# Kernel tuning notes

Hardware: AMD Instinct MI355X
Metric: run time of the kernel (lower is better)

Reference implementation:

```python
import jax, jax.numpy as jnp
import numpy as np

B, C, H, W = 256, 3, 224, 224
BRIGHT, CONTR, SATUR, HUE = 0.4, 0.4, 0.4, 0.1
ERASE_P = 0.25
PI = 3.14159


def _forward(x, flip_u, bj_u, cj_u, sj_u, hue_u, erase_u, area_u, aspect_u,
             top_u, left_u, erase_noise, mean, std):
    # uint8 -> float [0,1]
    xf = x.astype(jnp.float32) / 255.0
    # random horizontal flip (flip when rand > 0.5)
    flip = (flip_u > 0.5)[:, None, None, None]
    xf = jnp.where(flip, xf[..., ::-1], xf)
    # color jitter: brightness
    b_fac = 1.0 + (bj_u * 2.0 - 1.0) * BRIGHT
    xf = xf * b_fac
    # contrast
    c_fac = 1.0 + (cj_u * 2.0 - 1.0) * CONTR
    gray = xf.mean(axis=1, keepdims=True)
    xf = c_fac * xf + (1.0 - c_fac) * gray
    # saturation
    s_fac = 1.0 + (sj_u * 2.0 - 1.0) * SATUR
    gray = xf.mean(axis=1, keepdims=True)
    xf = s_fac * xf + (1.0 - s_fac) * gray
    # hue rotation
    h_fac = (hue_u * 2.0 - 1.0) * HUE * 0.5
    cos_h = jnp.cos(h_fac * PI)[:, None, None, None]
    sin_h = jnp.sin(h_fac * PI)[:, None, None, None]
    r, g, b = xf[:, 0:1], xf[:, 1:2], xf[:, 2:3]
    gray = (r + g + b) / 3.0
    xf = jnp.concatenate([
        gray + (r - gray) * cos_h + (g - b) * sin_h * 0.5,
        gray + (g - gray) * cos_h + (b - r) * sin_h * 0.5,
        gray + (b - gray) * cos_h + (r - g) * sin_h * 0.5,
    ], axis=1)
    xf = jnp.clip(xf, 0.0, 1.0)
    # normalize
    xf = (xf - mean) / std
    # vectorized random erasing
    area = float(H * W)
    target_area = (0.02 + area_u * (0.33 - 0.02)) * area          # [B]
    aspect = 0.3 + aspect_u * (3.3 - 0.3)                         # [B]
    h_e = jnp.round(jnp.sqrt(target_area * aspect)).astype(jnp.int32)
    w_e = jnp.round(jnp.sqrt(target_area / aspect)).astype(jnp.int32)
    apply = (erase_u < ERASE_P) & (h_e < H) & (w_e < W)           # [B]
    top = jnp.floor(top_u * jnp.maximum(H - h_e + 1, 1).astype(jnp.float32)).astype(jnp.int32)
    left = jnp.floor(left_u * jnp.maximum(W - w_e + 1, 1).astype(jnp.float32)).astype(jnp.int32)
    rows = jnp.arange(H)[None, :, None]   # [1,H,1]
    cols = jnp.arange(W)[None, None, :]   # [1,1,W]
    t = top[:, None, None]; l = left[:, None, None]
    he = h_e[:, None, None]; we = w_e[:, None, None]
    box = (rows >= t) & (rows < t + he) & (cols >= l) & (cols < l + we)  # [B,H,W]
    mask = (box & apply[:, None, None])[:, None, :, :]            # [B,1,H,W]
    xf = jnp.where(mask, erase_noise, xf)
    return xf


def setup_inputs() -> dict:
    key = jax.random.key(0)
    ks = jax.random.split(key, 14)
    return {
        "x": jax.random.randint(ks[0], (B, C, H, W), 0, 256, dtype=jnp.int32),
        "flip_u": jax.random.uniform(ks[1], (B,)),
        "bj_u": jax.random.uniform(ks[2], (B, 1, 1, 1)),
        "cj_u": jax.random.uniform(ks[3], (B, 1, 1, 1)),
        "sj_u": jax.random.uniform(ks[4], (B, 1, 1, 1)),
        "hue_u": jax.random.uniform(ks[5], (B,)),
        "erase_u": jax.random.uniform(ks[6], (B,)),
        "area_u": jax.random.uniform(ks[7], (B,)),
        "aspect_u": jax.random.uniform(ks[8], (B,)),
        "top_u": jax.random.uniform(ks[9], (B,)),
        "left_u": jax.random.uniform(ks[10], (B,)),
        "erase_noise": jax.random.normal(ks[11], (B, C, H, W), dtype=jnp.float32),
        "mean": jnp.array([0.485, 0.456, 0.406], dtype=jnp.float32).reshape(1, 3, 1, 1),
        "std": jnp.array([0.229, 0.224, 0.225], dtype=jnp.float32).reshape(1, 3, 1, 1),
    }


def reference(x, flip_u, bj_u, cj_u, sj_u, hue_u, erase_u, area_u, aspect_u,
              top_u, left_u, erase_noise, mean, std):
    return _forward(x, flip_u, bj_u, cj_u, sj_u, hue_u, erase_u, area_u,
                    aspect_u, top_u, left_u, erase_noise, mean, std)
```

## Files before the change

### kernel.cpp

```cpp
#include <hip/hip_runtime.h>
#include <math.h>

#define NB 256
#define NC 3
#define NH 224
#define NW 224
#define HW (NH * NW)
#define CHW (NC * HW)
#define GP 4
#define NT 256
#define WGR (NW / GP)
#define GPI (HW / GP)
#define BPI (GPI / NT)

struct __align__(16) Params {
    float b255;
    float k1;
    float k2;
    int   flip, apply, top, left, he, we;
};

__device__ inline void compute_params(int b,
    const float* __restrict__ flip_u, const float* __restrict__ bj_u,
    const float* __restrict__ cj_u,   const float* __restrict__ sj_u,
    const float* __restrict__ hue_u,  const float* __restrict__ erase_u,
    const float* __restrict__ area_u, const float* __restrict__ aspect_u,
    const float* __restrict__ top_u,  const float* __restrict__ left_u,
    Params* p)
{
#pragma clang fp contract(off)
    p->flip  = (flip_u[b] > 0.5f) ? 1 : 0;
    float b_fac = 1.0f + (bj_u[b] * 2.0f - 1.0f) * 0.4f;
    float c_fac = 1.0f + (cj_u[b] * 2.0f - 1.0f) * 0.4f;
    float s_fac = 1.0f + (sj_u[b] * 2.0f - 1.0f) * 0.4f;
    float h_fac = (hue_u[b] * 2.0f - 1.0f) * 0.1f * 0.5f;
    float ang   = h_fac * 3.14159f;
    float cs = c_fac * s_fac;
    p->b255 = b_fac * (1.0f / 255.0f);
    p->k1   = cs * cosf(ang);
    p->k2   = cs * sinf(ang) * 0.5f;

    float ta     = (0.02f + area_u[b] * 0.31f) * (float)HW;
    float aspect = 0.3f + aspect_u[b] * 3.0f;
    int he = (int)rintf(sqrtf(ta * aspect));
    int we = (int)rintf(sqrtf(ta / aspect));
    int apply = (erase_u[b] < 0.25f) && (he < NH) && (we < NW);
    int th = NH - he + 1; if (th < 1) th = 1;
    int tw = NW - we + 1; if (tw < 1) tw = 1;
    p->top  = (int)floorf(top_u[b]  * (float)th);
    p->left = (int)floorf(left_u[b] * (float)tw);
    p->he = he; p->we = we; p->apply = apply;
}

__global__ __launch_bounds__(NT) void aug_kernel(
    const int*   __restrict__ x,
    const float* __restrict__ flip_u, const float* __restrict__ bj_u,
    const float* __restrict__ cj_u,   const float* __restrict__ sj_u,
    const float* __restrict__ hue_u,  const float* __restrict__ erase_u,
    const float* __restrict__ area_u, const float* __restrict__ aspect_u,
    const float* __restrict__ top_u,  const float* __restrict__ left_u,
    const float* __restrict__ noise,  const float* __restrict__ mean,
    const float* __restrict__ stdv,
    float* __restrict__ out)
{
    __shared__ Params sp;
    __shared__ float sinv[3], smi[3];

    const int bimg = blockIdx.x / BPI;
    if (threadIdx.x == 0) {
        compute_params(bimg, flip_u, bj_u, cj_u, sj_u, hue_u, erase_u,
                       area_u, aspect_u, top_u, left_u, &sp);
        #pragma unroll
        for (int c = 0; c < 3; ++c) {
            float inv = 1.0f / stdv[c];
            sinv[c] = inv;
            smi[c]  = mean[c] * inv;
        }
    }
    __syncthreads();

    const int r  = (blockIdx.x % BPI) * NT + threadIdx.x;
    const int h  = r / WGR;
    const int w4 = (r - h * WGR) * GP;

    const int base  = bimg * CHW + h * NW;
    const int srcw4 = sp.flip ? (NW - GP - w4) : w4;

    int4 xi0 = *(const int4*)(x + base          + srcw4);
    int4 xi1 = *(const int4*)(x + base + HW     + srcw4);
    int4 xi2 = *(const int4*)(x + base + 2*HW   + srcw4);

    const float b255 = sp.b255, k1 = sp.k1, k2 = sp.k2;
    const float i0 = sinv[0], i1 = sinv[1], i2 = sinv[2];
    const float mi0 = smi[0], mi1 = smi[1], mi2 = smi[2];
    const float third = 1.0f / 3.0f;
    const int   flip = sp.flip;

    float v[3][GP];
    {
        const int* p0 = (const int*)&xi0;
        const int* p1 = (const int*)&xi1;
        const int* p2 = (const int*)&xi2;
        #pragma unroll
        for (int i = 0; i < GP; ++i) {
            const int src = flip ? (GP - 1 - i) : i;
            float r_ = (float)p0[src] * b255;
            float g_ = (float)p1[src] * b255;
            float b_ = (float)p2[src] * b255;

            float gray = (r_ + g_ + b_) * third;
            float rn = fmaf(k2, g_ - b_, fmaf(k1, r_ - gray, gray));
            float gn = fmaf(k2, b_ - r_, fmaf(k1, g_ - gray, gray));
            float bn = fmaf(k2, r_ - g_, fmaf(k1, b_ - gray, gray));

            rn = fminf(fmaxf(rn, 0.0f), 1.0f);
            gn = fminf(fmaxf(gn, 0.0f), 1.0f);
            bn = fminf(fmaxf(bn, 0.0f), 1.0f);

            v[0][i] = fmaf(rn, i0, -mi0);
            v[1][i] = fmaf(gn, i1, -mi1);
            v[2][i] = fmaf(bn, i2, -mi2);
        }
    }

    const bool rowin = sp.apply && (h >= sp.top) && (h < sp.top + sp.he);
    if (rowin) {
        #pragma unroll
        for (int i = 0; i < GP; ++i) {
            const int col = w4 + i;
            if (col >= sp.left && col < sp.left + sp.we) {
                v[0][i] = noise[base          + col];
                v[1][i] = noise[base + HW     + col];
                v[2][i] = noise[base + 2*HW   + col];
            }
        }
    }

    *(float4*)(out + base          + w4) = make_float4(v[0][0], v[0][1], v[0][2], v[0][3]);
    *(float4*)(out + base + HW     + w4) = make_float4(v[1][0], v[1][1], v[1][2], v[1][3]);
    *(float4*)(out + base + 2*HW   + w4) = make_float4(v[2][0], v[2][1], v[2][2], v[2][3]);
}

extern "C" void kernel_launch(void* const* d_in, const int* in_sizes, int n_in,
                              void* d_out, int out_size, void* d_ws, size_t ws_size,
                              hipStream_t stream) {
    const int*   x        = (const int*)  d_in[0];
    const float* flip_u   = (const float*)d_in[1];
    const float* bj_u     = (const float*)d_in[2];
    const float* cj_u     = (const float*)d_in[3];
    const float* sj_u     = (const float*)d_in[4];
    const float* hue_u    = (const float*)d_in[5];
    const float* erase_u  = (const float*)d_in[6];
    const float* area_u   = (const float*)d_in[7];
    const float* aspect_u = (const float*)d_in[8];
    const float* top_u    = (const float*)d_in[9];
    const float* left_u   = (const float*)d_in[10];
    const float* noise    = (const float*)d_in[11];
    const float* mean     = (const float*)d_in[12];
    const float* stdv     = (const float*)d_in[13];
    float* out = (float*)d_out;

    const int grid = NB * BPI;
    aug_kernel<<<grid, NT, 0, stream>>>(x, flip_u, bj_u, cj_u, sj_u, hue_u,
                                        erase_u, area_u, aspect_u, top_u, left_u,
                                        noise, mean, stdv, out);
}
```

Baseline: 60.85 us.

## Use persistent grid-stride blocks with software-prefetched next tile loads

Replaces the one-block-per-tile launch with 2048 persistent blocks that loop over virtual blocks. Each iteration loads the next tile's input ints before computing and storing the current one, so memory latency overlaps with compute. Per-image parameters are now computed redundantly by every thread instead of once per block through shared memory plus a barrier. The cost is more registers, extra scalar loads per thread, and possible load imbalance, since NVB/2048 is not an integer.

Result: no change. 61.88 us (+1.7%).

```diff
diff --git a/kernel.cpp b/kernel.cpp
--- a/kernel.cpp
+++ b/kernel.cpp
@@ -2,54 +2,56 @@
 #include <math.h>
 
 #define NB 256
-#define NC 3
 #define NH 224
 #define NW 224
 #define HW (NH * NW)
-#define CHW (NC * HW)
+#define CHW (3 * HW)
 #define GP 4
 #define NT 256
 #define WGR (NW / GP)
 #define GPI (HW / GP)
 #define BPI (GPI / NT)
+#define NVB (NB * BPI)
+#define PERSIST 2048
 
-struct __align__(16) Params {
+struct Params {
     float b255;
     float k1;
     float k2;
     int   flip, apply, top, left, he, we;
 };
 
-__device__ inline void compute_params(int b,
+__device__ __forceinline__ Params make_params(int b,
     const float* __restrict__ flip_u, const float* __restrict__ bj_u,
     const float* __restrict__ cj_u,   const float* __restrict__ sj_u,
     const float* __restrict__ hue_u,  const float* __restrict__ erase_u,
     const float* __restrict__ area_u, const float* __restrict__ aspect_u,
-    const float* __restrict__ top_u,  const float* __restrict__ left_u,
-    Params* p)
+    const float* __restrict__ top_u,  const float* __restrict__ left_u)
 {
 #pragma clang fp contract(off)
-    p->flip  = (flip_u[b] > 0.5f) ? 1 : 0;
+    Params p;
+    p.flip = (flip_u[b] > 0.5f) ? 1 : 0;
     float b_fac = 1.0f + (bj_u[b] * 2.0f - 1.0f) * 0.4f;
     float c_fac = 1.0f + (cj_u[b] * 2.0f - 1.0f) * 0.4f;
     float s_fac = 1.0f + (sj_u[b] * 2.0f - 1.0f) * 0.4f;
     float h_fac = (hue_u[b] * 2.0f - 1.0f) * 0.1f * 0.5f;
     float ang   = h_fac * 3.14159f;
     float cs = c_fac * s_fac;
-    p->b255 = b_fac * (1.0f / 255.0f);
-    p->k1   = cs * cosf(ang);
-    p->k2   = cs * sinf(ang) * 0.5f;
+    p.b255 = b_fac * (1.0f / 255.0f);
+    p.k1   = cs * cosf(ang);
+    p.k2   = cs * sinf(ang) * 0.5f;
 
     float ta     = (0.02f + area_u[b] * 0.31f) * (float)HW;
     float aspect = 0.3f + aspect_u[b] * 3.0f;
     int he = (int)rintf(sqrtf(ta * aspect));
     int we = (int)rintf(sqrtf(ta / aspect));
-    int apply = (erase_u[b] < 0.25f) && (he < NH) && (we < NW);
+    p.apply = (erase_u[b] < 0.25f) && (he < NH) && (we < NW);
     int th = NH - he + 1; if (th < 1) th = 1;
     int tw = NW - we + 1; if (tw < 1) tw = 1;
-    p->top  = (int)floorf(top_u[b]  * (float)th);
-    p->left = (int)floorf(left_u[b] * (float)tw);
-    p->he = he; p->we = we; p->apply = apply;
+    p.top  = (int)floorf(top_u[b]  * (float)th);
+    p.left = (int)floorf(left_u[b] * (float)tw);
+    p.he = he; p.we = we;
+    return p;
 }
 
 __global__ __launch_bounds__(NT) void aug_kernel(
@@ -63,82 +65,94 @@
     const float* __restrict__ stdv,
     float* __restrict__ out)
 {
-    __shared__ Params sp;
-    __shared__ float sinv[3], smi[3];
+    const float i0 = 1.0f / stdv[0], i1 = 1.0f / stdv[1], i2 = 1.0f / stdv[2];
+    const float mi0 = mean[0] * i0, mi1 = mean[1] * i1, mi2 = mean[2] * i2;
+    const float third = 1.0f / 3.0f;
+    const int tid = threadIdx.x;
 
-    const int bimg = blockIdx.x / BPI;
-    if (threadIdx.x == 0) {
-        compute_params(bimg, flip_u, bj_u, cj_u, sj_u, hue_u, erase_u,
-                       area_u, aspect_u, top_u, left_u, &sp);
-        #pragma unroll
-        for (int c = 0; c < 3; ++c) {
-            float inv = 1.0f / stdv[c];
-            sinv[c] = inv;
-            smi[c]  = mean[c] * inv;
-        }
-    }
-    __syncthreads();
+    auto geom = [&](unsigned vb, int flip, int& base, int& w4, int& h, int& srcw4) {
+        unsigned bimg = vb / BPI;
+        unsigned rblk = vb - bimg * BPI;
+        unsigned r  = rblk * NT + tid;
+        h  = (int)(r / WGR);
+        w4 = (int)(r - (unsigned)h * WGR) * GP;
+        base  = (int)bimg * CHW + h * NW;
+        srcw4 = flip ? (NW - GP - w4) : w4;
+    };
 
-    const int r  = (blockIdx.x % BPI) * NT + threadIdx.x;
-    const int h  = r / WGR;
-    const int w4 = (r - h * WGR) * GP;
-
-    const int base  = bimg * CHW + h * NW;
-    const int srcw4 = sp.flip ? (NW - GP - w4) : w4;
-
+    unsigned vb = blockIdx.x;
+    unsigned bimg = vb / BPI;
+    Params p = make_params((int)bimg, flip_u, bj_u, cj_u, sj_u, hue_u,
+                           erase_u, area_u, aspect_u, top_u, left_u);
+    int base, w4, h, srcw4;
+    geom(vb, p.flip, base, w4, h, srcw4);
     int4 xi0 = *(const int4*)(x + base          + srcw4);
     int4 xi1 = *(const int4*)(x + base + HW     + srcw4);
     int4 xi2 = *(const int4*)(x + base + 2*HW   + srcw4);
 
-    const float b255 = sp.b255, k1 = sp.k1, k2 = sp.k2;
-    const float i0 = sinv[0], i1 = sinv[1], i2 = sinv[2];
-    const float mi0 = smi[0], mi1 = smi[1], mi2 = smi[2];
-    const float third = 1.0f / 3.0f;
-    const int   flip = sp.flip;
+    for (;;) {
+        unsigned vbn = vb + PERSIST;
+        const bool last = (vbn >= NVB);
+        unsigned vbn_c = last ? vb : vbn;
+        unsigned bimg_n = vbn_c / BPI;
+        Params pn = make_params((int)bimg_n, flip_u, bj_u, cj_u, sj_u, hue_u,
+                                erase_u, area_u, aspect_u, top_u, left_u);
+        int base_n, w4_n, h_n, srcw4_n;
+        geom(vbn_c, pn.flip, base_n, w4_n, h_n, srcw4_n);
+        int4 yi0 = *(const int4*)(x + base_n          + srcw4_n);
+        int4 yi1 = *(const int4*)(x + base_n + HW     + srcw4_n);
+        int4 yi2 = *(const int4*)(x + base_n + 2*HW   + srcw4_n);
 
-    float v[3][GP];
-    {
-        const int* p0 = (const int*)&xi0;
-        const int* p1 = (const int*)&xi1;
-        const int* p2 = (const int*)&xi2;
-        #pragma unroll
-        for (int i = 0; i < GP; ++i) {
-            const int src = flip ? (GP - 1 - i) : i;
-            float r_ = (float)p0[src] * b255;
-            float g_ = (float)p1[src] * b255;
-            float b_ = (float)p2[src] * b255;
+        {
+            const float b255 = p.b255, k1 = p.k1, k2 = p.k2;
+            const int* p0 = (const int*)&xi0;
+            const int* p1 = (const int*)&xi1;
+            const int* p2 = (const int*)&xi2;
+            float v[3][GP];
+            #pragma unroll
+            for (int i = 0; i < GP; ++i) {
+                const int src = p.flip ? (GP - 1 - i) : i;
+                float r_ = (float)p0[src] * b255;
+                float g_ = (float)p1[src] * b255;
+                float b_ = (float)p2[src] * b255;
 
-            float gray = (r_ + g_ + b_) * third;
-            float rn = fmaf(k2, g_ - b_, fmaf(k1, r_ - gray, gray));
-            float gn = fmaf(k2, b_ - r_, fmaf(k1, g_ - gray, gray));
-            float bn = fmaf(k2, r_ - g_, fmaf(k1, b_ - gray, gray));
+                float gray = (r_ + g_ + b_) * third;
+                float rn = fmaf(k2, g_ - b_, fmaf(k1, r_ - gray, gray));
+                float gn = fmaf(k2, b_ - r_, fmaf(k1, g_ - gray, gray));
+                float bn = fmaf(k2, r_ - g_, fmaf(k1, b_ - gray, gray));
 
-            rn = fminf(fmaxf(rn, 0.0f), 1.0f);
-            gn = fminf(fmaxf(gn, 0.0f), 1.0f);
-            bn = fminf(fmaxf(bn, 0.0f), 1.0f);
+                rn = fminf(fmaxf(rn, 0.0f), 1.0f);
+                gn = fminf(fmaxf(gn, 0.0f), 1.0f);
+                bn = fminf(fmaxf(bn, 0.0f), 1.0f);
 
-            v[0][i] = fmaf(rn, i0, -mi0);
-            v[1][i] = fmaf(gn, i1, -mi1);
-            v[2][i] = fmaf(bn, i2, -mi2);
+                v[0][i] = fmaf(rn, i0, -mi0);
+                v[1][i] = fmaf(gn, i1, -mi1);
+                v[2][i] = fmaf(bn, i2, -mi2);
+            }
+
+            const bool rowin = p.apply && (h >= p.top) && (h < p.top + p.he);
+            if (rowin) {
+                #pragma unroll
+                for (int i = 0; i < GP; ++i) {
+                    const int col = w4 + i;
+                    if (col >= p.left && col < p.left + p.we) {
+                        v[0][i] = noise[base          + col];
+                        v[1][i] = noise[base + HW     + col];
+                        v[2][i] = noise[base + 2*HW   + col];
+                    }
+                }
+            }
+
+            *(float4*)(out + base          + w4) = make_float4(v[0][0], v[0][1], v[0][2], v[0][3]);
+            *(float4*)(out + base + HW     + w4) = make_float4(v[1][0], v[1][1], v[1][2], v[1][3]);
+            *(float4*)(out + base + 2*HW   + w4) = make_float4(v[2][0], v[2][1], v[2][2], v[2][3]);
         }
+
+        if (last) break;
+        vb = vbn; p = pn;
+        base = base_n; w4 = w4_n; h = h_n;
+        xi0 = yi0; xi1 = yi1; xi2 = yi2;
     }
-
-    const bool rowin = sp.apply && (h >= sp.top) && (h < sp.top + sp.he);
-    if (rowin) {
-        #pragma unroll
-        for (int i = 0; i < GP; ++i) {
-            const int col = w4 + i;
-            if (col >= sp.left && col < sp.left + sp.we) {
-                v[0][i] = noise[base          + col];
-                v[1][i] = noise[base + HW     + col];
-                v[2][i] = noise[base + 2*HW   + col];
-            }
-        }
-    }
-
-    *(float4*)(out + base          + w4) = make_float4(v[0][0], v[0][1], v[0][2], v[0][3]);
-    *(float4*)(out + base + HW     + w4) = make_float4(v[1][0], v[1][1], v[1][2], v[1][3]);
-    *(float4*)(out + base + 2*HW   + w4) = make_float4(v[2][0], v[2][1], v[2][2], v[2][3]);
 }
 
 extern "C" void kernel_launch(void* const* d_in, const int* in_sizes, int n_in,
@@ -160,8 +174,7 @@
     const float* stdv     = (const float*)d_in[13];
     float* out = (float*)d_out;
 
-    const int grid = NB * BPI;
-    aug_kernel<<<grid, NT, 0, stream>>>(x, flip_u, bj_u, cj_u, sj_u, hue_u,
-                                        erase_u, area_u, aspect_u, top_u, left_u,
-                                        noise, mean, stdv, out);
+    aug_kernel<<<PERSIST, NT, 0, stream>>>(x, flip_u, bj_u, cj_u, sj_u, hue_u,
+                                           erase_u, area_u, aspect_u, top_u, left_u,
+                                           noise, mean, stdv, out);
 }
```
